# Kernel tuning notes

Measured on AMD Instinct MI355X. Metric: run time of the kernel, lower is better.

Reference implementation:

```python
import jax, jax.numpy as jnp
import numpy as np
from jax import lax

B, L, D, H, DK, DFF, NL = 8, 128, 512, 8, 64, 2048, 6
T = 3 * L - 1
SC, AC = 14, 73  # state / action channel counts


def _linear(x, w, b):
    return x @ w.T + b


def _ln(x, w, b):
    m = x.mean(-1, keepdims=True)
    v = ((x - m) ** 2).mean(-1, keepdims=True)
    return (x - m) / jnp.sqrt(v + 1e-5) * w + b


def _conv(x, w, b):
    y = lax.conv_general_dilated(x, w, (1, 1), ((1, 1), (1, 1)),
                                 dimension_numbers=('NCHW', 'OIHW', 'NCHW'))
    return y + b[None, :, None, None]


def _convT(x, w, b, s, op):
    # torch ConvTranspose2d(k=3, stride=s, padding=1, output_padding=op)
    wt = jnp.flip(w, (2, 3)).transpose(1, 0, 2, 3)
    y = lax.conv_general_dilated(x, wt, (1, 1), ((1, 1 + op), (1, 1 + op)),
                                 lhs_dilation=(s, s),
                                 dimension_numbers=('NCHW', 'OIHW', 'NCHW'))
    return y + b[None, :, None, None]


def _cnn_enc(x, c1w, c1b, c2w, c2b, c3w, c3b, fcw, fcb, lnw, lnb):
    h = jax.nn.relu(_conv(x, c1w, c1b))
    h = jax.nn.relu(_conv(h, c2w, c2b))
    h = jax.nn.relu(_conv(h, c3w, c3b))
    h = h.reshape(h.shape[0], -1)
    return _ln(_linear(h, fcw, fcb), lnw, lnb)


def _mlp_enc(x, w1, b1, w2, b2, lnw, lnb):
    h = jax.nn.relu(_linear(x, w1, b1))
    return _ln(_linear(h, w2, b2), lnw, lnb)


def _decode(z, fcw, fcb, w1, b1, w2, b2, w3, b3):
    h = jax.nn.relu(_linear(z, fcw, fcb)).reshape(-1, 128, 2, 2)
    h = jax.nn.relu(_convT(h, w1, b1, 2, 1))
    h = jax.nn.relu(_convT(h, w2, b2, 2, 1))
    return _convT(h, w3, b3, 1, 0)


def setup_inputs():
    key = jax.random.key(0)
    cnt = [0]
    def nrm(shape, scale=0.02):
        cnt[0] += 1
        return jax.random.normal(jax.random.fold_in(key, cnt[0]), shape, jnp.float32) * scale
    z = lambda *s: jnp.zeros(s, jnp.float32)
    o = lambda *s: jnp.ones(s, jnp.float32)
    inp = dict(
        states=nrm((B, L, SC, 8, 8), 1.0),
        rtgs=nrm((B, L, 1), 1.0),
        timesteps=jax.random.randint(jax.random.fold_in(key, 9999), (B, L, 1), 0, 512, jnp.int32),
        actions=nrm((B, L - 1, AC, 8, 8), 1.0),
        mask=jnp.tril(jnp.ones((T, T), jnp.int32)),
        se_c1w=nrm((32, SC, 3, 3)), se_c1b=z(32),
        se_c2w=nrm((64, 32, 3, 3)), se_c2b=z(64),
        se_c3w=nrm((64, 64, 3, 3)), se_c3b=z(64),
        se_fcw=nrm((D, 64 * 64)), se_fcb=z(D), se_lnw=o(D), se_lnb=z(D),
        ae_c1w=nrm((32, AC, 3, 3)), ae_c1b=z(32),
        ae_c2w=nrm((64, 32, 3, 3)), ae_c2b=z(64),
        ae_c3w=nrm((64, 64, 3, 3)), ae_c3b=z(64),
        ae_fcw=nrm((D, 64 * 64)), ae_fcb=z(D), ae_lnw=o(D), ae_lnb=z(D),
        rtg_w1=nrm((D, 1)), rtg_b1=z(D), rtg_w2=nrm((D, D)), rtg_b2=z(D), rtg_lnw=o(D), rtg_lnb=z(D),
        ts_w1=nrm((D, 1)), ts_b1=z(D), ts_w2=nrm((D, D)), ts_b2=z(D), ts_lnw=o(D), ts_lnb=z(D),
        ip_w=nrm((D, D)), ip_b=z(D),
        lyr_wq=nrm((NL, D, D)), lyr_bq=z(NL, D),
        lyr_wk=nrm((NL, D, D)), lyr_bk=z(NL, D),
        lyr_wv=nrm((NL, D, D)), lyr_bv=z(NL, D),
        lyr_wo=nrm((NL, D, D)), lyr_bo=z(NL, D),
        lyr_f1w=nrm((NL, DFF, D)), lyr_f1b=z(NL, DFF),
        lyr_f2w=nrm((NL, D, DFF)), lyr_f2b=z(NL, D),
        lyr_l1w=o(NL, D), lyr_l1b=z(NL, D),
        lyr_l2w=o(NL, D), lyr_l2b=z(NL, D),
        ad_fcw=nrm((512, D)), ad_fcb=z(512),
        ad_w1=nrm((128, 64, 3, 3)), ad_b1=z(64),
        ad_w2=nrm((64, 32, 3, 3)), ad_b2=z(32),
        ad_w3=nrm((32, AC, 3, 3)), ad_b3=z(AC),
        sd_fcw=nrm((512, D)), sd_fcb=z(512),
        sd_w1=nrm((128, 64, 3, 3)), sd_b1=z(64),
        sd_w2=nrm((64, 32, 3, 3)), sd_b2=z(32),
        sd_w3=nrm((32, SC, 3, 3)), sd_b3=z(SC),
        rp_w=nrm((1, D)), rp_b=z(1),
    )
    return inp


def reference(states, rtgs, timesteps, actions, mask,
              se_c1w, se_c1b, se_c2w, se_c2b, se_c3w, se_c3b, se_fcw, se_fcb, se_lnw, se_lnb,
              ae_c1w, ae_c1b, ae_c2w, ae_c2b, ae_c3w, ae_c3b, ae_fcw, ae_fcb, ae_lnw, ae_lnb,
              rtg_w1, rtg_b1, rtg_w2, rtg_b2, rtg_lnw, rtg_lnb,
              ts_w1, ts_b1, ts_w2, ts_b2, ts_lnw, ts_lnb,
              ip_w, ip_b,
              lyr_wq, lyr_bq, lyr_wk, lyr_bk, lyr_wv, lyr_bv, lyr_wo, lyr_bo,
              lyr_f1w, lyr_f1b, lyr_f2w, lyr_f2b, lyr_l1w, lyr_l1b, lyr_l2w, lyr_l2b,
              ad_fcw, ad_fcb, ad_w1, ad_b1, ad_w2, ad_b2, ad_w3, ad_b3,
              sd_fcw, sd_fcb, sd_w1, sd_b1, sd_w2, sd_b2, sd_w3, sd_b3,
              rp_w, rp_b):
    b, l = states.shape[:2]
    s_emb = _cnn_enc(states.reshape(b * l, SC, 8, 8), se_c1w, se_c1b, se_c2w, se_c2b,
                     se_c3w, se_c3b, se_fcw, se_fcb, se_lnw, se_lnb).reshape(b, l, D)
    a_emb = _cnn_enc(actions.reshape(b * (l - 1), AC, 8, 8), ae_c1w, ae_c1b, ae_c2w, ae_c2b,
                     ae_c3w, ae_c3b, ae_fcw, ae_fcb, ae_lnw, ae_lnb).reshape(b, l - 1, D)
    r_emb = _mlp_enc(rtgs.reshape(b * l, 1), rtg_w1, rtg_b1, rtg_w2, rtg_b2, rtg_lnw, rtg_lnb).reshape(b, l, D)
    t_emb = _mlp_enc(timesteps.astype(jnp.float32).reshape(b * l, 1), ts_w1, ts_b1, ts_w2, ts_b2, ts_lnw, ts_lnb).reshape(b, l, D)
    # interleave (rtg, state, action) tokens -> length 3L-1
    comb = jnp.zeros((b, 3 * l - 1, D), jnp.float32)
    comb = comb.at[:, 0::3].set(r_emb + t_emb)
    comb = comb.at[:, 1::3].set(s_emb + t_emb)
    comb = comb.at[:, 2::3].set(a_emb + t_emb[:, :-1])
    x = _linear(comb, ip_w, ip_b)  # dropout is identity in eval
    keep = (mask != 0)[None, None]
    scale = 1.0 / float(np.sqrt(DK))

    def block(x, p):
        wq, bq, wk, bk, wv, bv, wo, bo, f1w, f1b, f2w, f2b, l1w, l1b, l2w, l2b = p
        t = x.shape[1]
        q = _linear(x, wq, bq).reshape(b, t, H, DK).transpose(0, 2, 1, 3)
        k = _linear(x, wk, bk).reshape(b, t, H, DK).transpose(0, 2, 1, 3)
        v = _linear(x, wv, bv).reshape(b, t, H, DK).transpose(0, 2, 1, 3)
        sc = jnp.einsum('bhqd,bhkd->bhqk', q, k) * scale
        sc = jnp.where(keep, sc, jnp.float32(-1e9))
        att = jax.nn.softmax(sc, axis=-1)
        o = jnp.einsum('bhqk,bhkd->bhqd', att, v).transpose(0, 2, 1, 3).reshape(b, t, D)
        x = _ln(x + _linear(o, wo, bo), l1w, l1b)
        ff = _linear(jax.nn.relu(_linear(x, f1w, f1b)), f2w, f2b)
        x = _ln(x + ff, l2w, l2b)
        return x, None

    x, _ = lax.scan(block, x, (lyr_wq, lyr_bq, lyr_wk, lyr_bk, lyr_wv, lyr_bv, lyr_wo, lyr_bo,
                               lyr_f1w, lyr_f1b, lyr_f2w, lyr_f2b, lyr_l1w, lyr_l1b, lyr_l2w, lyr_l2b))
    x_state = x[:, ::3]
    x_action = x[:, 1::3]
    x_reward = x[:, 2::3]
    action_preds = _decode(x_action.reshape(-1, D), ad_fcw, ad_fcb, ad_w1, ad_b1, ad_w2, ad_b2, ad_w3, ad_b3).reshape(b, -1, AC, 8, 8)
    state_preds = _decode(x_state.reshape(-1, D), sd_fcw, sd_fcb, sd_w1, sd_b1, sd_w2, sd_b2, sd_w3, sd_b3).reshape(b, -1, SC, 8, 8)
    reward_preds = _linear(x_reward, rp_w, rp_b)
    return action_preds, state_preds, reward_preds
```

## Files before the change

kernel.cpp:

```cpp
#include <hip/hip_runtime.h>


#define TT 383

typedef short      bf16x8 __attribute__((ext_vector_type(8)));
typedef float      f32x4  __attribute__((ext_vector_type(4)));
typedef unsigned short u16x8 __attribute__((ext_vector_type(8)));
typedef unsigned short u16x4 __attribute__((ext_vector_type(4)));

__device__ __forceinline__ unsigned short f2bf(float f)
{
  unsigned u = __float_as_uint(f);
  return (unsigned short)((u + 0x7FFFu + ((u >> 16) & 1u)) >> 16);
}

__global__ __launch_bounds__(256) void cast_bf16_kernel(
    const float* __restrict__ in, unsigned short* __restrict__ out, long n)
{
  long i = ((long)blockIdx.x * 256 + threadIdx.x) * 4;
  if (i >= n) return;
  const float4 v = *(const float4*)(in + i);
  u16x4 o;
  o.x = f2bf(v.x); o.y = f2bf(v.y); o.z = f2bf(v.z); o.w = f2bf(v.w);
  *(u16x4*)(out + i) = o;
}

#define LDAP 72
__global__ __launch_bounds__(256) void gemm_bf16_kernel(
    const unsigned short* __restrict__ A, const unsigned short* __restrict__ B,
    const float* __restrict__ bias, float* __restrict__ C,
    int M, int N, int K, int relu, int obf)
{
  __shared__ __align__(16) unsigned short As[128 * LDAP];
  __shared__ __align__(16) unsigned short Bs[128 * LDAP];

  const int tid = threadIdx.x;
  const int lane = tid & 63;
  const int w  = tid >> 6;
  const int wr = w >> 1, wc = w & 1;
  const int m0 = blockIdx.x * 128, n0 = blockIdx.y * 128;

  const int lr = lane & 15;
  const int hi = lane >> 4;

  f32x4 acc[4][4] = {};

  const int r = tid >> 1;
  const int h = tid & 1;

  int mrow = m0 + r; if (mrow >= M) mrow = M - 1;
  const unsigned short* Ap = A + (long)mrow * K + h * 32;
  const unsigned short* Bp = B + (long)(n0 + r) * K + h * 32;
  unsigned short* Asd = As + r * LDAP + h * 32;
  unsigned short* Bsd = Bs + r * LDAP + h * 32;

  for (int k0 = 0; k0 < K; k0 += 64) {
#pragma unroll
    for (int i = 0; i < 4; ++i)
      *(u16x8*)(Asd + i * 8) = *(const u16x8*)(Ap + k0 + i * 8);
#pragma unroll
    for (int i = 0; i < 4; ++i)
      *(u16x8*)(Bsd + i * 8) = *(const u16x8*)(Bp + k0 + i * 8);
    __syncthreads();

#pragma unroll
    for (int kk = 0; kk < 2; ++kk) {
      const int kof = kk * 32 + hi * 8;
      bf16x8 a[4], b[4];
#pragma unroll
      for (int t = 0; t < 4; ++t)
        a[t] = *(const bf16x8*)(As + (wr * 64 + t * 16 + lr) * LDAP + kof);
#pragma unroll
      for (int t = 0; t < 4; ++t)
        b[t] = *(const bf16x8*)(Bs + (wc * 64 + t * 16 + lr) * LDAP + kof);
#pragma unroll
      for (int i = 0; i < 4; ++i)
#pragma unroll
        for (int j = 0; j < 4; ++j)
          acc[i][j] = __builtin_amdgcn_mfma_f32_16x16x32_bf16(a[i], b[j], acc[i][j], 0, 0, 0);
    }
    __syncthreads();
  }

#pragma unroll
  for (int j = 0; j < 4; ++j) {
    const int col = n0 + wc * 64 + j * 16 + lr;
    const float bv = bias ? bias[col] : 0.f;
#pragma unroll
    for (int i = 0; i < 4; ++i) {
#pragma unroll
      for (int v = 0; v < 4; ++v) {
        int row = m0 + wr * 64 + i * 16 + hi * 4 + v;
        if (row < M) {
          float x = acc[i][j][v] + bv;
          if (relu) x = fmaxf(x, 0.f);
          if (obf) ((unsigned short*)C)[(long)row * N + col] = f2bf(x);
          else     C[(long)row * N + col] = x;
        }
      }
    }
  }
}

static inline void gemm_bf(hipStream_t st, const unsigned short* A, const unsigned short* B,
                           const float* bias, float* C, int M, int N, int K,
                           int relu = 0, int obf = 0)
{
  dim3 g((M + 127) / 128, N / 128);
  gemm_bf16_kernel<<<g, 256, 0, st>>>(A, B, bias, C, M, N, K, relu, obf);
}

static inline void cast_bf(hipStream_t st, const float* in, unsigned short* out, long n)
{
  cast_bf16_kernel<<<(int)((n / 4 + 255) / 256), 256, 0, st>>>(in, out, n);
}

__global__ __launch_bounds__(256) void attn_kernel(
    const unsigned short* __restrict__ Qb, const unsigned short* __restrict__ Kb,
    const unsigned short* __restrict__ Vb, unsigned short* __restrict__ Ob)
{
  __shared__ __align__(16) unsigned short Kl[32 * 72];
  __shared__ __align__(16) unsigned short Vt[64 * 40];
  __shared__ __align__(16) unsigned short Pl[4][16 * 40];

  const int tid = threadIdx.x;
  const int lane = tid & 63;
  const int w = tid >> 6;
  const int lr = lane & 15, hi = lane >> 4;
  const int q0 = blockIdx.x * 64;
  const int bh = blockIdx.y;
  const int b = bh >> 3, h = bh & 7;
  const long base = (long)b * TT * 512 + h * 64;

  const int qrow = q0 + w * 16 + lr;
  const int qr_c = qrow < TT ? qrow : TT - 1;
  bf16x8 qf0 = *(const bf16x8*)(Qb + base + (long)qr_c * 512 + hi * 8);
  bf16x8 qf1 = *(const bf16x8*)(Qb + base + (long)qr_c * 512 + 32 + hi * 8);

  float m[4], l[4];
  f32x4 acc[4];
#pragma unroll
  for (int r = 0; r < 4; ++r) { m[r] = -1e30f; l[r] = 0.f; }
#pragma unroll
  for (int c = 0; c < 4; ++c) acc[c] = (f32x4){0.f, 0.f, 0.f, 0.f};

  const int qmax = min(q0 + 63, TT - 1);
  const int nkv = qmax + 1;

  for (int kv0 = 0; kv0 < nkv; kv0 += 32) {
    __syncthreads();
    {
      int e = tid * 8;
      int kv = e >> 6, d = e & 63;
      int skv = kv0 + kv; if (skv >= TT) skv = TT - 1;
      *(u16x8*)(Kl + kv * 72 + d) = *(const u16x8*)(Kb + base + (long)skv * 512 + d);
      u16x8 vv = *(const u16x8*)(Vb + base + (long)skv * 512 + d);
#pragma unroll
      for (int j = 0; j < 8; ++j) Vt[(d + j) * 40 + kv] = vv[j];
    }
    __syncthreads();

    f32x4 s[2] = {};
#pragma unroll
    for (int t = 0; t < 2; ++t) {
      bf16x8 k0 = *(const bf16x8*)(Kl + (t * 16 + lr) * 72 + hi * 8);
      bf16x8 k1 = *(const bf16x8*)(Kl + (t * 16 + lr) * 72 + 32 + hi * 8);
      s[t] = __builtin_amdgcn_mfma_f32_16x16x32_bf16(qf0, k0, s[t], 0, 0, 0);
      s[t] = __builtin_amdgcn_mfma_f32_16x16x32_bf16(qf1, k1, s[t], 0, 0, 0);
    }

    const int qq = q0 + w * 16 + hi * 4;
#pragma unroll
    for (int r = 0; r < 4; ++r) {
      float v0 = s[0][r] * 0.125f;
      float v1 = s[1][r] * 0.125f;
      const int qr = qq + r;
      const int kvA = kv0 + lr, kvB = kv0 + 16 + lr;
      if (kvA > qr || kvA >= TT) v0 = -1e30f;
      if (kvB > qr || kvB >= TT) v1 = -1e30f;
      float rm = fmaxf(v0, v1);
      rm = fmaxf(rm, __shfl_xor(rm, 1));
      rm = fmaxf(rm, __shfl_xor(rm, 2));
      rm = fmaxf(rm, __shfl_xor(rm, 4));
      rm = fmaxf(rm, __shfl_xor(rm, 8));
      float mn = fmaxf(m[r], rm);
      float al = expf(m[r] - mn);
      float e0 = expf(v0 - mn);
      float e1 = expf(v1 - mn);
      float rs = e0 + e1;
      rs += __shfl_xor(rs, 1);
      rs += __shfl_xor(rs, 2);
      rs += __shfl_xor(rs, 4);
      rs += __shfl_xor(rs, 8);
      l[r] = l[r] * al + rs;
      m[r] = mn;
#pragma unroll
      for (int c = 0; c < 4; ++c) acc[c][r] *= al;
      Pl[w][(hi * 4 + r) * 40 + lr]      = f2bf(e0);
      Pl[w][(hi * 4 + r) * 40 + 16 + lr] = f2bf(e1);
    }

    bf16x8 pa = *(const bf16x8*)(&Pl[w][lr * 40 + hi * 8]);
#pragma unroll
    for (int c = 0; c < 4; ++c) {
      bf16x8 vf = *(const bf16x8*)(Vt + (c * 16 + lr) * 40 + hi * 8);
      acc[c] = __builtin_amdgcn_mfma_f32_16x16x32_bf16(pa, vf, acc[c], 0, 0, 0);
    }
  }

  float inv[4];
#pragma unroll
  for (int r = 0; r < 4; ++r) inv[r] = 1.0f / l[r];
#pragma unroll
  for (int c = 0; c < 4; ++c) {
#pragma unroll
    for (int r = 0; r < 4; ++r) {
      int qr = q0 + w * 16 + hi * 4 + r;
      if (qr < TT) Ob[base + (long)qr * 512 + c * 16 + lr] = f2bf(acc[c][r] * inv[r]);
    }
  }
}

template <int CIN>
__global__ __launch_bounds__(256) void conv3x3_kernel(
    const float* __restrict__ in, const float* __restrict__ w,
    const float* __restrict__ bias, float* __restrict__ out, int Cout)
{
  __shared__ float img[CIN * 100];
  const int n = blockIdx.x;
  const int tid = threadIdx.x;
  for (int i = tid; i < CIN * 100; i += 256) img[i] = 0.f;
  __syncthreads();
  const float* src = in + (long)n * CIN * 64;
  for (int i = tid; i < CIN * 64; i += 256) {
    int ic = i >> 6, p = i & 63;
    img[ic * 100 + ((p >> 3) + 1) * 10 + (p & 7) + 1] = src[i];
  }
  __syncthreads();

  const int y  = tid & 7;
  const int oc = blockIdx.y * 32 + (tid >> 3);
  if (oc >= Cout) return;

  float acc[8];
#pragma unroll
  for (int x = 0; x < 8; ++x) acc[x] = bias[oc];

  const float* wp = w + (long)oc * CIN * 9;
  for (int ic = 0; ic < CIN; ++ic) {
    float wr[9];
#pragma unroll
    for (int q = 0; q < 9; ++q) wr[q] = wp[ic * 9 + q];
    const float* ib = &img[ic * 100 + y * 10];
#pragma unroll
    for (int ky = 0; ky < 3; ++ky) {
      const float* r = ib + ky * 10;
      float c0 = r[0], c1 = r[1];
#pragma unroll
      for (int x = 0; x < 8; ++x) {
        float c2 = r[x + 2];
        acc[x] = fmaf(c0, wr[ky * 3 + 0],
                 fmaf(c1, wr[ky * 3 + 1],
                 fmaf(c2, wr[ky * 3 + 2], acc[x])));
        c0 = c1; c1 = c2;
      }
    }
  }
  float* dst = out + ((long)n * Cout + oc) * 64 + y * 8;
#pragma unroll
  for (int x = 0; x < 8; ++x) dst[x] = fmaxf(acc[x], 0.f);
}

template <int CIN, int IH, int S, int OP, int OH>
__global__ __launch_bounds__(256) void convT_fast_kernel(
    const float* __restrict__ in, const float* __restrict__ w,
    const float* __restrict__ bias, float* __restrict__ out,
    int Cout, int relu)
{
  constexpr int DW = (IH - 1) * S + 3 + OP;
  constexpr int OCPB = 256 / OH;
  __shared__ float img[CIN * DW * DW];

  const int n = blockIdx.x;
  const int tid = threadIdx.x;
  for (int i = tid; i < CIN * DW * DW; i += 256) img[i] = 0.f;
  __syncthreads();
  const float* src = in + (long)n * CIN * IH * IH;
  for (int i = tid; i < CIN * IH * IH; i += 256) {
    int ic = i / (IH * IH), p = i % (IH * IH);
    int iy = p / IH, ix = p % IH;
    img[ic * DW * DW + (1 + iy * S) * DW + (1 + ix * S)] = src[i];
  }
  __syncthreads();

  const int y  = tid % OH;
  const int oc = blockIdx.y * OCPB + tid / OH;
  if (oc >= Cout) return;

  float acc[OH];
#pragma unroll
  for (int x = 0; x < OH; ++x) acc[x] = bias[oc];

  for (int ic = 0; ic < CIN; ++ic) {
    const float* wp = w + ((long)ic * Cout + oc) * 9;
    float wr[9];
#pragma unroll
    for (int q = 0; q < 9; ++q) wr[q] = wp[8 - q];
    const float* ib = &img[ic * DW * DW + y * DW];
#pragma unroll
    for (int ky = 0; ky < 3; ++ky) {
      const float* r = ib + ky * DW;
      float c0 = r[0], c1 = r[1];
#pragma unroll
      for (int x = 0; x < OH; ++x) {
        float c2 = r[x + 2];
        acc[x] = fmaf(c0, wr[ky * 3 + 0],
                 fmaf(c1, wr[ky * 3 + 1],
                 fmaf(c2, wr[ky * 3 + 2], acc[x])));
        c0 = c1; c1 = c2;
      }
    }
  }
  float* dst = out + ((long)n * Cout + oc) * OH * OH + y * OH;
#pragma unroll
  for (int x = 0; x < OH; ++x) dst[x] = relu ? fmaxf(acc[x], 0.f) : acc[x];
}

__device__ __forceinline__ float blockReduceSum256(float v)
{
  __shared__ float sb[4];
  int lane = threadIdx.x & 63, wid = threadIdx.x >> 6;
#pragma unroll
  for (int o = 32; o; o >>= 1) v += __shfl_down(v, o);
  __syncthreads();
  if (lane == 0) sb[wid] = v;
  __syncthreads();
  return sb[0] + sb[1] + sb[2] + sb[3];
}

__global__ __launch_bounds__(256) void add_ln_kernel(
    const float* __restrict__ a, const float* __restrict__ b,
    const float* __restrict__ w, const float* __restrict__ bb,
    float* __restrict__ out)
{
  long row = blockIdx.x;
  const float* pa = a + row * 512;
  float x0 = pa[threadIdx.x], x1 = pa[threadIdx.x + 256];
  if (b) {
    const float* pb = b + row * 512;
    x0 += pb[threadIdx.x]; x1 += pb[threadIdx.x + 256];
  }
  float mean = blockReduceSum256(x0 + x1) * (1.f / 512.f);
  float d0 = x0 - mean, d1 = x1 - mean;
  float var = blockReduceSum256(d0 * d0 + d1 * d1) * (1.f / 512.f);
  float inv = 1.0f / sqrtf(var + 1e-5f);
  float* po = out + row * 512;
  po[threadIdx.x]       = d0 * inv * w[threadIdx.x] + bb[threadIdx.x];
  po[threadIdx.x + 256] = d1 * inv * w[threadIdx.x + 256] + bb[threadIdx.x + 256];
}

__global__ void lin1_relu_kernel(const float* __restrict__ x, const float* __restrict__ w,
                                 const float* __restrict__ b, float* __restrict__ out, long total)
{
  long idx = (long)blockIdx.x * 256 + threadIdx.x;
  if (idx >= total) return;
  int d = idx & 511; long r = idx >> 9;
  out[idx] = fmaxf(fmaf(x[r], w[d], b[d]), 0.f);
}

__global__ void lin1_relu_int_kernel(const int* __restrict__ x, const float* __restrict__ w,
                                     const float* __restrict__ b, float* __restrict__ out, long total)
{
  long idx = (long)blockIdx.x * 256 + threadIdx.x;
  if (idx >= total) return;
  int d = idx & 511; long r = idx >> 9;
  out[idx] = fmaxf(fmaf((float)x[r], w[d], b[d]), 0.f);
}

__global__ void build_comb_kernel(const float* __restrict__ r, const float* __restrict__ s,
                                  const float* __restrict__ a, const float* __restrict__ t,
                                  float* __restrict__ comb)
{
  long idx = (long)blockIdx.x * 256 + threadIdx.x;
  if (idx >= (long)8 * TT * 512) return;
  int d = idx & 511;
  long rr = idx >> 9;
  int tok = (int)(rr % TT);
  int b   = (int)(rr / TT);
  int grp = tok / 3, ph = tok % 3;
  float te = t[((long)b * 128 + grp) * 512 + d];
  float v;
  if (ph == 0)      v = r[((long)b * 128 + grp) * 512 + d] + te;
  else if (ph == 1) v = s[((long)b * 128 + grp) * 512 + d] + te;
  else              v = a[((long)b * 127 + grp) * 512 + d] + te;
  comb[idx] = v;
}

__global__ void gather3_kernel(const float* __restrict__ x, float* __restrict__ out,
                               int offset, int count)
{
  long idx = (long)blockIdx.x * 256 + threadIdx.x;
  long total = (long)8 * count * 512;
  if (idx >= total) return;
  int d = idx & 511;
  long r = idx >> 9;
  int i = (int)(r % count);
  int b = (int)(r / count);
  out[idx] = x[((long)b * TT + offset + 3 * i) * 512 + d];
}

__global__ __launch_bounds__(256) void reward_kernel(const float* __restrict__ x,
                                                     const float* __restrict__ w,
                                                     const float* __restrict__ b,
                                                     float* __restrict__ out, int rows)
{
  int row = blockIdx.x * 4 + (threadIdx.x >> 6);
  int lane = threadIdx.x & 63;
  if (row >= rows) return;
  const float* p = x + (long)row * 512;
  float s = 0.f;
  for (int j = lane; j < 512; j += 64) s = fmaf(p[j], w[j], s);
#pragma unroll
  for (int o = 32; o; o >>= 1) s += __shfl_xor(s, o);
  if (lane == 0) out[row] = s + b[0];
}

extern "C" void kernel_launch(void* const* d_in, const int* in_sizes, int n_in,
                              void* d_out, int out_size, void* d_ws, size_t ws_size,
                              hipStream_t stream)
{
  const float* states  = (const float*)d_in[0];
  const float* rtgs    = (const float*)d_in[1];
  const int*   tsteps  = (const int*)d_in[2];
  const float* actions = (const float*)d_in[3];
  const float* se_c1w = (const float*)d_in[5];  const float* se_c1b = (const float*)d_in[6];
  const float* se_c2w = (const float*)d_in[7];  const float* se_c2b = (const float*)d_in[8];
  const float* se_c3w = (const float*)d_in[9];  const float* se_c3b = (const float*)d_in[10];
  const float* se_fcw = (const float*)d_in[11]; const float* se_fcb = (const float*)d_in[12];
  const float* se_lnw = (const float*)d_in[13]; const float* se_lnb = (const float*)d_in[14];
  const float* ae_c1w = (const float*)d_in[15]; const float* ae_c1b = (const float*)d_in[16];
  const float* ae_c2w = (const float*)d_in[17]; const float* ae_c2b = (const float*)d_in[18];
  const float* ae_c3w = (const float*)d_in[19]; const float* ae_c3b = (const float*)d_in[20];
  const float* ae_fcw = (const float*)d_in[21]; const float* ae_fcb = (const float*)d_in[22];
  const float* ae_lnw = (const float*)d_in[23]; const float* ae_lnb = (const float*)d_in[24];
  const float* rtg_w1 = (const float*)d_in[25]; const float* rtg_b1 = (const float*)d_in[26];
  const float* rtg_w2 = (const float*)d_in[27]; const float* rtg_b2 = (const float*)d_in[28];
  const float* rtg_lnw= (const float*)d_in[29]; const float* rtg_lnb= (const float*)d_in[30];
  const float* ts_w1  = (const float*)d_in[31]; const float* ts_b1  = (const float*)d_in[32];
  const float* ts_w2  = (const float*)d_in[33]; const float* ts_b2  = (const float*)d_in[34];
  const float* ts_lnw = (const float*)d_in[35]; const float* ts_lnb = (const float*)d_in[36];
  const float* ip_w   = (const float*)d_in[37]; const float* ip_b   = (const float*)d_in[38];
  const float* lyr_wq = (const float*)d_in[39]; const float* lyr_bq = (const float*)d_in[40];
  const float* lyr_wk = (const float*)d_in[41]; const float* lyr_bk = (const float*)d_in[42];
  const float* lyr_wv = (const float*)d_in[43]; const float* lyr_bv = (const float*)d_in[44];
  const float* lyr_wo = (const float*)d_in[45]; const float* lyr_bo = (const float*)d_in[46];
  const float* lyr_f1w= (const float*)d_in[47]; const float* lyr_f1b= (const float*)d_in[48];
  const float* lyr_f2w= (const float*)d_in[49]; const float* lyr_f2b= (const float*)d_in[50];
  const float* lyr_l1w= (const float*)d_in[51]; const float* lyr_l1b= (const float*)d_in[52];
  const float* lyr_l2w= (const float*)d_in[53]; const float* lyr_l2b= (const float*)d_in[54];
  const float* ad_fcw = (const float*)d_in[55]; const float* ad_fcb = (const float*)d_in[56];
  const float* ad_w1  = (const float*)d_in[57]; const float* ad_b1  = (const float*)d_in[58];
  const float* ad_w2  = (const float*)d_in[59]; const float* ad_b2  = (const float*)d_in[60];
  const float* ad_w3  = (const float*)d_in[61]; const float* ad_b3  = (const float*)d_in[62];
  const float* sd_fcw = (const float*)d_in[63]; const float* sd_fcb = (const float*)d_in[64];
  const float* sd_w1  = (const float*)d_in[65]; const float* sd_b1  = (const float*)d_in[66];
  const float* sd_w2  = (const float*)d_in[67]; const float* sd_b2  = (const float*)d_in[68];
  const float* sd_w3  = (const float*)d_in[69]; const float* sd_b3  = (const float*)d_in[70];
  const float* rp_w   = (const float*)d_in[71]; const float* rp_b   = (const float*)d_in[72];

  float* ws = (float*)d_ws;
  long off = 0;
  auto alloc = [&](long n) { float* p = ws + off; off += n; return p; };

  float* region = alloc(10485760);
  float* h1 = region;
  float* h2 = region + 2097152;
  float* h3 = region + 6291456;
  float* s_emb = alloc(524288);
  float* a_emb = alloc(520192);
  float* r_emb = alloc(524288);
  float* t_emb = alloc(524288);
  float* etmp  = alloc(524288);
  float* xa = alloc(1568768);
  float* xb = alloc(1568768);
  float* qb = alloc(1568768);
  float* kb = alloc(1568768);
  float* vb = alloc(1568768);
  float* t2 = alloc(1568768);
  float* ffh = alloc(6275072);

  unsigned short* qbh = (unsigned short*)qb;
  unsigned short* kbh = (unsigned short*)kb;
  unsigned short* vbh = (unsigned short*)vb;

  unsigned short* bws = (unsigned short*)(ws + off);
  long boff = 0;
  auto ballo = [&](long n) { unsigned short* p = bws + boff; boff += n; return p; };
  unsigned short* ipW  = ballo(262144);
  unsigned short* wqW  = ballo(6L * 262144);
  unsigned short* wkW  = ballo(6L * 262144);
  unsigned short* wvW  = ballo(6L * 262144);
  unsigned short* woW  = ballo(6L * 262144);
  unsigned short* f1W  = ballo(6L * 1048576);
  unsigned short* f2W  = ballo(6L * 1048576);
  unsigned short* seW  = ballo(2097152);
  unsigned short* aeW  = ballo(2097152);
  unsigned short* rtgW = ballo(262144);
  unsigned short* tsW  = ballo(262144);
  unsigned short* adW  = ballo(262144);
  unsigned short* sdW  = ballo(262144);
  unsigned short* abuf = ballo(6275072);

  const long BT = (long)8 * TT;

  cast_bf(stream, ip_w,    ipW,  262144);
  cast_bf(stream, lyr_wq,  wqW,  6L * 262144);
  cast_bf(stream, lyr_wk,  wkW,  6L * 262144);
  cast_bf(stream, lyr_wv,  wvW,  6L * 262144);
  cast_bf(stream, lyr_wo,  woW,  6L * 262144);
  cast_bf(stream, lyr_f1w, f1W,  6L * 1048576);
  cast_bf(stream, lyr_f2w, f2W,  6L * 1048576);
  cast_bf(stream, se_fcw,  seW,  2097152);
  cast_bf(stream, ae_fcw,  aeW,  2097152);
  cast_bf(stream, rtg_w2,  rtgW, 262144);
  cast_bf(stream, ts_w2,   tsW,  262144);
  cast_bf(stream, ad_fcw,  adW,  262144);
  cast_bf(stream, sd_fcw,  sdW,  262144);

  conv3x3_kernel<14><<<dim3(1024, 1), 256, 0, stream>>>(states, se_c1w, se_c1b, h1, 32);
  conv3x3_kernel<32><<<dim3(1024, 2), 256, 0, stream>>>(h1, se_c2w, se_c2b, h2, 64);
  conv3x3_kernel<64><<<dim3(1024, 2), 256, 0, stream>>>(h2, se_c3w, se_c3b, h3, 64);
  cast_bf(stream, h3, abuf, 1024L * 4096);
  gemm_bf(stream, abuf, seW, se_fcb, etmp, 1024, 512, 4096);
  add_ln_kernel<<<1024, 256, 0, stream>>>(etmp, nullptr, se_lnw, se_lnb, s_emb);

  conv3x3_kernel<73><<<dim3(1016, 1), 256, 0, stream>>>(actions, ae_c1w, ae_c1b, h1, 32);
  conv3x3_kernel<32><<<dim3(1016, 2), 256, 0, stream>>>(h1, ae_c2w, ae_c2b, h2, 64);
  conv3x3_kernel<64><<<dim3(1016, 2), 256, 0, stream>>>(h2, ae_c3w, ae_c3b, h3, 64);
  cast_bf(stream, h3, abuf, 1016L * 4096);
  gemm_bf(stream, abuf, aeW, ae_fcb, etmp, 1016, 512, 4096);
  add_ln_kernel<<<1016, 256, 0, stream>>>(etmp, nullptr, ae_lnw, ae_lnb, a_emb);

  lin1_relu_kernel<<<(1024 * 512 + 255) / 256, 256, 0, stream>>>(rtgs, rtg_w1, rtg_b1, qb, 1024 * 512);
  cast_bf(stream, qb, abuf, 1024L * 512);
  gemm_bf(stream, abuf, rtgW, rtg_b2, etmp, 1024, 512, 512);
  add_ln_kernel<<<1024, 256, 0, stream>>>(etmp, nullptr, rtg_lnw, rtg_lnb, r_emb);

  lin1_relu_int_kernel<<<(1024 * 512 + 255) / 256, 256, 0, stream>>>(tsteps, ts_w1, ts_b1, qb, 1024 * 512);
  cast_bf(stream, qb, abuf, 1024L * 512);
  gemm_bf(stream, abuf, tsW, ts_b2, etmp, 1024, 512, 512);
  add_ln_kernel<<<1024, 256, 0, stream>>>(etmp, nullptr, ts_lnw, ts_lnb, t_emb);

  build_comb_kernel<<<(int)((8L * TT * 512 + 255) / 256), 256, 0, stream>>>(r_emb, s_emb, a_emb, t_emb, xb);
  cast_bf(stream, xb, abuf, BT * 512);
  gemm_bf(stream, abuf, ipW, ip_b, xa, (int)BT, 512, 512);

  for (int l = 0; l < 6; ++l) {
    const unsigned short* wq = wqW + (long)l * 262144; const float* bq = lyr_bq + (long)l * 512;
    const unsigned short* wk = wkW + (long)l * 262144; const float* bk = lyr_bk + (long)l * 512;
    const unsigned short* wv = wvW + (long)l * 262144; const float* bv = lyr_bv + (long)l * 512;
    const unsigned short* wo = woW + (long)l * 262144; const float* bo = lyr_bo + (long)l * 512;
    const unsigned short* f1w = f1W + (long)l * 1048576; const float* f1b = lyr_f1b + (long)l * 2048;
    const unsigned short* f2w = f2W + (long)l * 1048576; const float* f2b = lyr_f2b + (long)l * 512;
    const float* l1w = lyr_l1w + (long)l * 512; const float* l1b = lyr_l1b + (long)l * 512;
    const float* l2w = lyr_l2w + (long)l * 512; const float* l2b = lyr_l2b + (long)l * 512;

    cast_bf(stream, xa, abuf, BT * 512);
    gemm_bf(stream, abuf, wq, bq, (float*)qbh, (int)BT, 512, 512, 0, 1);
    gemm_bf(stream, abuf, wk, bk, (float*)kbh, (int)BT, 512, 512, 0, 1);
    gemm_bf(stream, abuf, wv, bv, (float*)vbh, (int)BT, 512, 512, 0, 1);

    attn_kernel<<<dim3(6, 64), 256, 0, stream>>>(qbh, kbh, vbh, abuf);

    gemm_bf(stream, abuf, wo, bo, t2, (int)BT, 512, 512);
    add_ln_kernel<<<(int)BT, 256, 0, stream>>>(xa, t2, l1w, l1b, xb);
    cast_bf(stream, xb, abuf, BT * 512);
    gemm_bf(stream, abuf, f1w, f1b, ffh, (int)BT, 2048, 512, 1);
    cast_bf(stream, ffh, abuf, BT * 2048);
    gemm_bf(stream, abuf, f2w, f2b, t2, (int)BT, 512, 2048);
    add_ln_kernel<<<(int)BT, 256, 0, stream>>>(xb, t2, l2w, l2b, xa);
  }

  float* outp = (float*)d_out;
  float* act_out = outp;
  float* st_out  = outp + 4784128;
  float* rw_out  = outp + 5701632;

  float* za  = region;
  float* zfc = region + 524288;
  float* dh1 = region + 1048576;
  float* dh2 = region + 2097152;

  gather3_kernel<<<(1024 * 512 + 255) / 256, 256, 0, stream>>>(xa, za, 1, 128);
  cast_bf(stream, za, abuf, 1024L * 512);
  gemm_bf(stream, abuf, adW, ad_fcb, zfc, 1024, 512, 512, 1);
  convT_fast_kernel<128, 2, 2, 1, 4><<<dim3(1024, 1), 256, 0, stream>>>(zfc, ad_w1, ad_b1, dh1, 64, 1);
  convT_fast_kernel<64, 4, 2, 1, 8><<<dim3(1024, 1), 256, 0, stream>>>(dh1, ad_w2, ad_b2, dh2, 32, 1);
  convT_fast_kernel<32, 8, 1, 0, 8><<<dim3(1024, 3), 256, 0, stream>>>(dh2, ad_w3, ad_b3, act_out, 73, 0);

  gather3_kernel<<<(1024 * 512 + 255) / 256, 256, 0, stream>>>(xa, za, 0, 128);
  cast_bf(stream, za, abuf, 1024L * 512);
  gemm_bf(stream, abuf, sdW, sd_fcb, zfc, 1024, 512, 512, 1);
  convT_fast_kernel<128, 2, 2, 1, 4><<<dim3(1024, 1), 256, 0, stream>>>(zfc, sd_w1, sd_b1, dh1, 64, 1);
  convT_fast_kernel<64, 4, 2, 1, 8><<<dim3(1024, 1), 256, 0, stream>>>(dh1, sd_w2, sd_b2, dh2, 32, 1);
  convT_fast_kernel<32, 8, 1, 0, 8><<<dim3(1024, 1), 256, 0, stream>>>(dh2, sd_w3, sd_b3, st_out, 14, 0);

  gather3_kernel<<<(1016 * 512 + 255) / 256, 256, 0, stream>>>(xa, za, 2, 127);
  reward_kernel<<<(1016 + 3) / 4, 256, 0, stream>>>(za, rp_w, rp_b, rw_out, 1016);
}
```

Baseline: 2.435 ms.

## Fuse QKV projection, split-K narrow GEMMs, emit bf16 from layernorm

Merges the Q/K/V weights into one 1536-wide GEMM and has attention read the interleaved QKV buffer. Adds split-K with atomic float accumulation for the N=512 GEMMs, including the 4096-deep embedding FCs, to raise occupancy. Layernorm and the FFN1 GEMM now write bf16 directly, which removes separate cast kernels. Decoder FC ReLU is moved into the convT input load so it survives split-K. The cost is extra memsets and atomics, plus a non-deterministic summation order.

Measured after the change: 2.058 ms. 1.18x faster.

```diff
diff --git a/kernel.cpp b/kernel.cpp
--- a/kernel.cpp
+++ b/kernel.cpp
@@ -25,11 +25,37 @@
   *(u16x4*)(out + i) = o;
 }
 
+__global__ __launch_bounds__(256) void merge_qkv_w_kernel(
+    const float* __restrict__ wq, const float* __restrict__ wk,
+    const float* __restrict__ wv, unsigned short* __restrict__ dst)
+{
+  long i = ((long)blockIdx.x * 256 + threadIdx.x) * 4;
+  if (i >= 6L * 786432) return;
+  long l = i / 786432, rem = i % 786432;
+  int which = (int)(rem / 262144);
+  long o = rem % 262144;
+  const float* src = which == 0 ? wq : which == 1 ? wk : wv;
+  float4 v = *(const float4*)(src + l * 262144 + o);
+  u16x4 w;
+  w.x = f2bf(v.x); w.y = f2bf(v.y); w.z = f2bf(v.z); w.w = f2bf(v.w);
+  *(u16x4*)(dst + i) = w;
+}
+
+__global__ void merge_qkv_b_kernel(const float* __restrict__ bq, const float* __restrict__ bk,
+                                   const float* __restrict__ bv, float* __restrict__ dst)
+{
+  int i = blockIdx.x * 256 + threadIdx.x;
+  if (i >= 6 * 1536) return;
+  int l = i / 1536, r = i % 1536;
+  int which = r >> 9, o = r & 511;
+  dst[i] = (which == 0 ? bq : which == 1 ? bk : bv)[l * 512 + o];
+}
+
 #define LDAP 72
 __global__ __launch_bounds__(256) void gemm_bf16_kernel(
     const unsigned short* __restrict__ A, const unsigned short* __restrict__ B,
     const float* __restrict__ bias, float* __restrict__ C,
-    int M, int N, int K, int relu, int obf)
+    int M, int N, int K, int relu, int obf, int splitK)
 {
   __shared__ __align__(16) unsigned short As[128 * LDAP];
   __shared__ __align__(16) unsigned short Bs[128 * LDAP];
@@ -39,6 +65,7 @@
   const int w  = tid >> 6;
   const int wr = w >> 1, wc = w & 1;
   const int m0 = blockIdx.x * 128, n0 = blockIdx.y * 128;
+  const int z  = blockIdx.z;
 
   const int lr = lane & 15;
   const int hi = lane >> 4;
@@ -54,7 +81,10 @@
   unsigned short* Asd = As + r * LDAP + h * 32;
   unsigned short* Bsd = Bs + r * LDAP + h * 32;
 
-  for (int k0 = 0; k0 < K; k0 += 64) {
+  const int kLen = K / splitK;
+  const int kBeg = z * kLen, kEnd = kBeg + kLen;
+
+  for (int k0 = kBeg; k0 < kEnd; k0 += 64) {
 #pragma unroll
     for (int i = 0; i < 4; ++i)
       *(u16x8*)(Asd + i * 8) = *(const u16x8*)(Ap + k0 + i * 8);
@@ -85,7 +115,7 @@
 #pragma unroll
   for (int j = 0; j < 4; ++j) {
     const int col = n0 + wc * 64 + j * 16 + lr;
-    const float bv = bias ? bias[col] : 0.f;
+    const float bv = (bias && z == 0) ? bias[col] : 0.f;
 #pragma unroll
     for (int i = 0; i < 4; ++i) {
 #pragma unroll
@@ -93,9 +123,13 @@
         int row = m0 + wr * 64 + i * 16 + hi * 4 + v;
         if (row < M) {
           float x = acc[i][j][v] + bv;
-          if (relu) x = fmaxf(x, 0.f);
-          if (obf) ((unsigned short*)C)[(long)row * N + col] = f2bf(x);
-          else     C[(long)row * N + col] = x;
+          if (splitK > 1) {
+            atomicAdd(&C[(long)row * N + col], x);
+          } else {
+            if (relu) x = fmaxf(x, 0.f);
+            if (obf) ((unsigned short*)C)[(long)row * N + col] = f2bf(x);
+            else     C[(long)row * N + col] = x;
+          }
         }
       }
     }
@@ -106,8 +140,16 @@
                            const float* bias, float* C, int M, int N, int K,
                            int relu = 0, int obf = 0)
 {
-  dim3 g((M + 127) / 128, N / 128);
-  gemm_bf16_kernel<<<g, 256, 0, st>>>(A, B, bias, C, M, N, K, relu, obf);
+  dim3 g((M + 127) / 128, N / 128, 1);
+  gemm_bf16_kernel<<<g, 256, 0, st>>>(A, B, bias, C, M, N, K, relu, obf, 1);
+}
+
+static inline void gemm_sk(hipStream_t st, const unsigned short* A, const unsigned short* B,
+                           const float* bias, float* C, int M, int N, int K, int S)
+{
+  hipMemsetAsync(C, 0, (size_t)M * N * 4, st);
+  dim3 g((M + 127) / 128, N / 128, S);
+  gemm_bf16_kernel<<<g, 256, 0, st>>>(A, B, bias, C, M, N, K, 0, 0, S);
 }
 
 static inline void cast_bf(hipStream_t st, const float* in, unsigned short* out, long n)
@@ -116,8 +158,7 @@
 }
 
 __global__ __launch_bounds__(256) void attn_kernel(
-    const unsigned short* __restrict__ Qb, const unsigned short* __restrict__ Kb,
-    const unsigned short* __restrict__ Vb, unsigned short* __restrict__ Ob)
+    const unsigned short* __restrict__ Qkv, unsigned short* __restrict__ Ob)
 {
   __shared__ __align__(16) unsigned short Kl[32 * 72];
   __shared__ __align__(16) unsigned short Vt[64 * 40];
@@ -130,12 +171,13 @@
   const int q0 = blockIdx.x * 64;
   const int bh = blockIdx.y;
   const int b = bh >> 3, h = bh & 7;
-  const long base = (long)b * TT * 512 + h * 64;
+  const long baseq = (long)b * TT * 1536 + h * 64;
+  const long baseo = (long)b * TT * 512 + h * 64;
 
   const int qrow = q0 + w * 16 + lr;
   const int qr_c = qrow < TT ? qrow : TT - 1;
-  bf16x8 qf0 = *(const bf16x8*)(Qb + base + (long)qr_c * 512 + hi * 8);
-  bf16x8 qf1 = *(const bf16x8*)(Qb + base + (long)qr_c * 512 + 32 + hi * 8);
+  bf16x8 qf0 = *(const bf16x8*)(Qkv + baseq + (long)qr_c * 1536 + hi * 8);
+  bf16x8 qf1 = *(const bf16x8*)(Qkv + baseq + (long)qr_c * 1536 + 32 + hi * 8);
 
   float m[4], l[4];
   f32x4 acc[4];
@@ -153,8 +195,8 @@
       int e = tid * 8;
       int kv = e >> 6, d = e & 63;
       int skv = kv0 + kv; if (skv >= TT) skv = TT - 1;
-      *(u16x8*)(Kl + kv * 72 + d) = *(const u16x8*)(Kb + base + (long)skv * 512 + d);
-      u16x8 vv = *(const u16x8*)(Vb + base + (long)skv * 512 + d);
+      *(u16x8*)(Kl + kv * 72 + d) = *(const u16x8*)(Qkv + baseq + 512 + (long)skv * 1536 + d);
+      u16x8 vv = *(const u16x8*)(Qkv + baseq + 1024 + (long)skv * 1536 + d);
 #pragma unroll
       for (int j = 0; j < 8; ++j) Vt[(d + j) * 40 + kv] = vv[j];
     }
@@ -216,7 +258,7 @@
 #pragma unroll
     for (int r = 0; r < 4; ++r) {
       int qr = q0 + w * 16 + hi * 4 + r;
-      if (qr < TT) Ob[base + (long)qr * 512 + c * 16 + lr] = f2bf(acc[c][r] * inv[r]);
+      if (qr < TT) Ob[baseo + (long)qr * 512 + c * 16 + lr] = f2bf(acc[c][r] * inv[r]);
     }
   }
 }
@@ -275,7 +317,7 @@
 __global__ __launch_bounds__(256) void convT_fast_kernel(
     const float* __restrict__ in, const float* __restrict__ w,
     const float* __restrict__ bias, float* __restrict__ out,
-    int Cout, int relu)
+    int Cout, int relu, int inRelu)
 {
   constexpr int DW = (IH - 1) * S + 3 + OP;
   constexpr int OCPB = 256 / OH;
@@ -289,7 +331,9 @@
   for (int i = tid; i < CIN * IH * IH; i += 256) {
     int ic = i / (IH * IH), p = i % (IH * IH);
     int iy = p / IH, ix = p % IH;
-    img[ic * DW * DW + (1 + iy * S) * DW + (1 + ix * S)] = src[i];
+    float v = src[i];
+    if (inRelu) v = fmaxf(v, 0.f);
+    img[ic * DW * DW + (1 + iy * S) * DW + (1 + ix * S)] = v;
   }
   __syncthreads();
 
@@ -341,7 +385,7 @@
 __global__ __launch_bounds__(256) void add_ln_kernel(
     const float* __restrict__ a, const float* __restrict__ b,
     const float* __restrict__ w, const float* __restrict__ bb,
-    float* __restrict__ out)
+    float* __restrict__ out, unsigned short* __restrict__ outbf)
 {
   long row = blockIdx.x;
   const float* pa = a + row * 512;
@@ -354,9 +398,15 @@
   float d0 = x0 - mean, d1 = x1 - mean;
   float var = blockReduceSum256(d0 * d0 + d1 * d1) * (1.f / 512.f);
   float inv = 1.0f / sqrtf(var + 1e-5f);
+  float v0 = d0 * inv * w[threadIdx.x] + bb[threadIdx.x];
+  float v1 = d1 * inv * w[threadIdx.x + 256] + bb[threadIdx.x + 256];
   float* po = out + row * 512;
-  po[threadIdx.x]       = d0 * inv * w[threadIdx.x] + bb[threadIdx.x];
-  po[threadIdx.x + 256] = d1 * inv * w[threadIdx.x + 256] + bb[threadIdx.x + 256];
+  po[threadIdx.x]       = v0;
+  po[threadIdx.x + 256] = v1;
+  if (outbf) {
+    outbf[row * 512 + threadIdx.x]       = f2bf(v0);
+    outbf[row * 512 + threadIdx.x + 256] = f2bf(v1);
+  }
 }
 
 __global__ void lin1_relu_kernel(const float* __restrict__ x, const float* __restrict__ w,
@@ -483,40 +533,35 @@
   float* etmp  = alloc(524288);
   float* xa = alloc(1568768);
   float* xb = alloc(1568768);
-  float* qb = alloc(1568768);
-  float* kb = alloc(1568768);
-  float* vb = alloc(1568768);
   float* t2 = alloc(1568768);
-  float* ffh = alloc(6275072);
-
-  unsigned short* qbh = (unsigned short*)qb;
-  unsigned short* kbh = (unsigned short*)kb;
-  unsigned short* vbh = (unsigned short*)vb;
+  float* qkvB = alloc(9216);
 
   unsigned short* bws = (unsigned short*)(ws + off);
   long boff = 0;
   auto ballo = [&](long n) { unsigned short* p = bws + boff; boff += n; return p; };
-  unsigned short* ipW  = ballo(262144);
-  unsigned short* wqW  = ballo(6L * 262144);
-  unsigned short* wkW  = ballo(6L * 262144);
-  unsigned short* wvW  = ballo(6L * 262144);
-  unsigned short* woW  = ballo(6L * 262144);
-  unsigned short* f1W  = ballo(6L * 1048576);
-  unsigned short* f2W  = ballo(6L * 1048576);
-  unsigned short* seW  = ballo(2097152);
-  unsigned short* aeW  = ballo(2097152);
-  unsigned short* rtgW = ballo(262144);
-  unsigned short* tsW  = ballo(262144);
-  unsigned short* adW  = ballo(262144);
-  unsigned short* sdW  = ballo(262144);
-  unsigned short* abuf = ballo(6275072);
+  unsigned short* ipW   = ballo(262144);
+  unsigned short* wqkvW = ballo(6L * 786432);
+  unsigned short* woW   = ballo(6L * 262144);
+  unsigned short* f1W   = ballo(6L * 1048576);
+  unsigned short* f2W   = ballo(6L * 1048576);
+  unsigned short* seW   = ballo(2097152);
+  unsigned short* aeW   = ballo(2097152);
+  unsigned short* rtgW  = ballo(262144);
+  unsigned short* tsW   = ballo(262144);
+  unsigned short* adW   = ballo(262144);
+  unsigned short* sdW   = ballo(262144);
+  unsigned short* qkvbf = ballo(4706304);
+  unsigned short* aobf  = ballo(1568768);
+  unsigned short* xbfA  = ballo(1568768);
+  unsigned short* xbfB  = ballo(1568768);
+  unsigned short* ffhbf = ballo(6275072);
+  unsigned short* abuf  = ballo(6275072);
 
   const long BT = (long)8 * TT;
 
   cast_bf(stream, ip_w,    ipW,  262144);
-  cast_bf(stream, lyr_wq,  wqW,  6L * 262144);
-  cast_bf(stream, lyr_wk,  wkW,  6L * 262144);
-  cast_bf(stream, lyr_wv,  wvW,  6L * 262144);
+  merge_qkv_w_kernel<<<(int)((6L * 786432 / 4 + 255) / 256), 256, 0, stream>>>(lyr_wq, lyr_wk, lyr_wv, wqkvW);
+  merge_qkv_b_kernel<<<(6 * 1536 + 255) / 256, 256, 0, stream>>>(lyr_bq, lyr_bk, lyr_bv, qkvB);
   cast_bf(stream, lyr_wo,  woW,  6L * 262144);
   cast_bf(stream, lyr_f1w, f1W,  6L * 1048576);
   cast_bf(stream, lyr_f2w, f2W,  6L * 1048576);
@@ -531,54 +576,47 @@
   conv3x3_kernel<32><<<dim3(1024, 2), 256, 0, stream>>>(h1, se_c2w, se_c2b, h2, 64);
   conv3x3_kernel<64><<<dim3(1024, 2), 256, 0, stream>>>(h2, se_c3w, se_c3b, h3, 64);
   cast_bf(stream, h3, abuf, 1024L * 4096);
-  gemm_bf(stream, abuf, seW, se_fcb, etmp, 1024, 512, 4096);
-  add_ln_kernel<<<1024, 256, 0, stream>>>(etmp, nullptr, se_lnw, se_lnb, s_emb);
+  gemm_sk(stream, abuf, seW, se_fcb, etmp, 1024, 512, 4096, 8);
+  add_ln_kernel<<<1024, 256, 0, stream>>>(etmp, nullptr, se_lnw, se_lnb, s_emb, nullptr);
 
   conv3x3_kernel<73><<<dim3(1016, 1), 256, 0, stream>>>(actions, ae_c1w, ae_c1b, h1, 32);
   conv3x3_kernel<32><<<dim3(1016, 2), 256, 0, stream>>>(h1, ae_c2w, ae_c2b, h2, 64);
   conv3x3_kernel<64><<<dim3(1016, 2), 256, 0, stream>>>(h2, ae_c3w, ae_c3b, h3, 64);
   cast_bf(stream, h3, abuf, 1016L * 4096);
-  gemm_bf(stream, abuf, aeW, ae_fcb, etmp, 1016, 512, 4096);
-  add_ln_kernel<<<1016, 256, 0, stream>>>(etmp, nullptr, ae_lnw, ae_lnb, a_emb);
-
-  lin1_relu_kernel<<<(1024 * 512 + 255) / 256, 256, 0, stream>>>(rtgs, rtg_w1, rtg_b1, qb, 1024 * 512);
-  cast_bf(stream, qb, abuf, 1024L * 512);
-  gemm_bf(stream, abuf, rtgW, rtg_b2, etmp, 1024, 512, 512);
-  add_ln_kernel<<<1024, 256, 0, stream>>>(etmp, nullptr, rtg_lnw, rtg_lnb, r_emb);
-
-  lin1_relu_int_kernel<<<(1024 * 512 + 255) / 256, 256, 0, stream>>>(tsteps, ts_w1, ts_b1, qb, 1024 * 512);
-  cast_bf(stream, qb, abuf, 1024L * 512);
-  gemm_bf(stream, abuf, tsW, ts_b2, etmp, 1024, 512, 512);
-  add_ln_kernel<<<1024, 256, 0, stream>>>(etmp, nullptr, ts_lnw, ts_lnb, t_emb);
+  gemm_sk(stream, abuf, aeW, ae_fcb, etmp, 1016, 512, 4096, 8);
+  add_ln_kernel<<<1016, 256, 0, stream>>>(etmp, nullptr, ae_lnw, ae_lnb, a_emb, nullptr);
+
+  lin1_relu_kernel<<<(1024 * 512 + 255) / 256, 256, 0, stream>>>(rtgs, rtg_w1, rtg_b1, t2, 1024 * 512);
+  cast_bf(stream, t2, abuf, 1024L * 512);
+  gemm_sk(stream, abuf, rtgW, rtg_b2, etmp, 1024, 512, 512, 8);
+  add_ln_kernel<<<1024, 256, 0, stream>>>(etmp, nullptr, rtg_lnw, rtg_lnb, r_emb, nullptr);
+
+  lin1_relu_int_kernel<<<(1024 * 512 + 255) / 256, 256, 0, stream>>>(tsteps, ts_w1, ts_b1, t2, 1024 * 512);
+  cast_bf(stream, t2, abuf, 1024L * 512);
+  gemm_sk(stream, abuf, tsW, ts_b2, etmp, 1024, 512, 512, 8);
+  add_ln_kernel<<<1024, 256, 0, stream>>>(etmp, nullptr, ts_lnw, ts_lnb, t_emb, nullptr);
 
   build_comb_kernel<<<(int)((8L * TT * 512 + 255) / 256), 256, 0, stream>>>(r_emb, s_emb, a_emb, t_emb, xb);
   cast_bf(stream, xb, abuf, BT * 512);
-  gemm_bf(stream, abuf, ipW, ip_b, xa, (int)BT, 512, 512);
+  gemm_sk(stream, abuf, ipW, ip_b, xa, (int)BT, 512, 512, 4);
+  cast_bf(stream, xa, xbfA, BT * 512);
 
   for (int l = 0; l < 6; ++l) {
-    const unsigned short* wq = wqW + (long)l * 262144; const float* bq = lyr_bq + (long)l * 512;
-    const unsigned short* wk = wkW + (long)l * 262144; const float* bk = lyr_bk + (long)l * 512;
-    const unsigned short* wv = wvW + (long)l * 262144; const float* bv = lyr_bv + (long)l * 512;
+    const unsigned short* wqkv = wqkvW + (long)l * 786432;
+    const float* bqkv = qkvB + (long)l * 1536;
     const unsigned short* wo = woW + (long)l * 262144; const float* bo = lyr_bo + (long)l * 512;
     const unsigned short* f1w = f1W + (long)l * 1048576; const float* f1b = lyr_f1b + (long)l * 2048;
     const unsigned short* f2w = f2W + (long)l * 1048576; const float* f2b = lyr_f2b + (long)l * 512;
     const float* l1w = lyr_l1w + (long)l * 512; const float* l1b = lyr_l1b + (long)l * 512;
     const float* l2w = lyr_l2w + (long)l * 512; const float* l2b = lyr_l2b + (long)l * 512;
 
-    cast_bf(stream, xa, abuf, BT * 512);
-    gemm_bf(stream, abuf, wq, bq, (float*)qbh, (int)BT, 512, 512, 0, 1);
-    gemm_bf(stream, abuf, wk, bk, (float*)kbh, (int)BT, 512, 512, 0, 1);
-    gemm_bf(stream, abuf, wv, bv, (float*)vbh, (int)BT, 512, 512, 0, 1);
-
-    attn_kernel<<<dim3(6, 64), 256, 0, stream>>>(qbh, kbh, vbh, abuf);
-
-    gemm_bf(stream, abuf, wo, bo, t2, (int)BT, 512, 512);
-    add_ln_kernel<<<(int)BT, 256, 0, stream>>>(xa, t2, l1w, l1b, xb);
-    cast_bf(stream, xb, abuf, BT * 512);
-    gemm_bf(stream, abuf, f1w, f1b, ffh, (int)BT, 2048, 512, 1);
-    cast_bf(stream, ffh, abuf, BT * 2048);
-    gemm_bf(stream, abuf, f2w, f2b, t2, (int)BT, 512, 2048);
-    add_ln_kernel<<<(int)BT, 256, 0, stream>>>(xb, t2, l2w, l2b, xa);
+    gemm_bf(stream, xbfA, wqkv, bqkv, (float*)qkvbf, (int)BT, 1536, 512, 0, 1);
+    attn_kernel<<<dim3(6, 64), 256, 0, stream>>>(qkvbf, aobf);
+    gemm_sk(stream, aobf, wo, bo, t2, (int)BT, 512, 512, 4);
+    add_ln_kernel<<<(int)BT, 256, 0, stream>>>(xa, t2, l1w, l1b, xb, xbfB);
+    gemm_bf(stream, xbfB, f1w, f1b, (float*)ffhbf, (int)BT, 2048, 512, 1, 1);
+    gemm_sk(stream, ffhbf, f2w, f2b, t2, (int)BT, 512, 2048, 4);
+    add_ln_kernel<<<(int)BT, 256, 0, stream>>>(xb, t2, l2w, l2b, xa, xbfA);
   }
 
   float* outp = (float*)d_out;
@@ -593,17 +631,17 @@
 
   gather3_kernel<<<(1024 * 512 + 255) / 256, 256, 0, stream>>>(xa, za, 1, 128);
   cast_bf(stream, za, abuf, 1024L * 512);
-  gemm_bf(stream, abuf, adW, ad_fcb, zfc, 1024, 512, 512, 1);
-  convT_fast_kernel<128, 2, 2, 1, 4><<<dim3(1024, 1), 256, 0, stream>>>(zfc, ad_w1, ad_b1, dh1, 64, 1);
-  convT_fast_kernel<64, 4, 2, 1, 8><<<dim3(1024, 1), 256, 0, stream>>>(dh1, ad_w2, ad_b2, dh2, 32, 1);
-  convT_fast_kernel<32, 8, 1, 0, 8><<<dim3(1024, 3), 256, 0, stream>>>(dh2, ad_w3, ad_b3, act_out, 73, 0);
+  gemm_sk(stream, abuf, adW, ad_fcb, zfc, 1024, 512, 512, 8);
+  convT_fast_kernel<128, 2, 2, 1, 4><<<dim3(1024, 1), 256, 0, stream>>>(zfc, ad_w1, ad_b1, dh1, 64, 1, 1);
+  convT_fast_kernel<64, 4, 2, 1, 8><<<dim3(1024, 1), 256, 0, stream>>>(dh1, ad_w2, ad_b2, dh2, 32, 1, 0);
+  convT_fast_kernel<32, 8, 1, 0, 8><<<dim3(1024, 3), 256, 0, stream>>>(dh2, ad_w3, ad_b3, act_out, 73, 0, 0);
 
   gather3_kernel<<<(1024 * 512 + 255) / 256, 256, 0, stream>>>(xa, za, 0, 128);
   cast_bf(stream, za, abuf, 1024L * 512);
-  gemm_bf(stream, abuf, sdW, sd_fcb, zfc, 1024, 512, 512, 1);
-  convT_fast_kernel<128, 2, 2, 1, 4><<<dim3(1024, 1), 256, 0, stream>>>(zfc, sd_w1, sd_b1, dh1, 64, 1);
-  convT_fast_kernel<64, 4, 2, 1, 8><<<dim3(1024, 1), 256, 0, stream>>>(dh1, sd_w2, sd_b2, dh2, 32, 1);
-  convT_fast_kernel<32, 8, 1, 0, 8><<<dim3(1024, 1), 256, 0, stream>>>(dh2, sd_w3, sd_b3, st_out, 14, 0);
+  gemm_sk(stream, abuf, sdW, sd_fcb, zfc, 1024, 512, 512, 8);
+  convT_fast_kernel<128, 2, 2, 1, 4><<<dim3(1024, 1), 256, 0, stream>>>(zfc, sd_w1, sd_b1, dh1, 64, 1, 1);
+  convT_fast_kernel<64, 4, 2, 1, 8><<<dim3(1024, 1), 256, 0, stream>>>(dh1, sd_w2, sd_b2, dh2, 32, 1, 0);
+  convT_fast_kernel<32, 8, 1, 0, 8><<<dim3(1024, 1), 256, 0, stream>>>(dh2, sd_w3, sd_b3, st_out, 14, 0, 0);
 
   gather3_kernel<<<(1016 * 512 + 255) / 256, 256, 0, stream>>>(xa, za, 2, 127);
   reward_kernel<<<(1016 + 3) / 4, 256, 0, stream>>>(za, rp_w, rp_b, rw_out, 1016);
```
